# Kernel optimization log

Hardware: AMD Instinct MI355X
Metric: run time of the kernel (lower is better)

Reference implementation:

```python
import jax, jax.numpy as jnp
import numpy as np

RATE = 22050.0 / 256.0
_RANGES = [(0.0, 0.32537674), (0.32537674, 0.47555801), (0.47555801, 0.64588683),
           (0.64588683, 1.16883525), (1.16883525, 2.17128976), (2.17128976, np.inf)]
LO = np.array([a * RATE for a, _ in _RANGES], dtype=np.float32)
HI = np.array([b * RATE for _, b in _RANGES], dtype=np.float32)
WEIGHT = 1.0
EPS = 1e-7


def _giou1d(a0, a1, b0, b1):
    # 1D GIoU between intervals [a0,a1] (GT) and [b0,b1] (pred)
    inter = jnp.clip(jnp.minimum(a1, b1) - jnp.maximum(a0, b0), 0.0)
    union = (a1 - a0) + (b1 - b0) - inter
    enclose = jnp.maximum(a1, b1) - jnp.minimum(a0, b0)
    iou = inter / (union + EPS)
    return iou - (enclose - union) / (enclose + EPS)


def _fcos_loss(regressions, annotations, anchor_levels):
    # anchor_levels: list of 6 1D point arrays. All annotations are valid and
    # belong to class_id, so the boolean class filters are identity (jit-safe).
    def per_sample(reg, ann):
        # sort GTs by interval length ascending (as in get_fcos_positives)
        order = jnp.argsort(ann[:, 1] - ann[:, 0])
        ann = ann[order]  # [G, 3]
        losses, pos_masks = [], []
        off = 0
        for i, pts in enumerate(anchor_levels):
            n = pts.shape[0]
            reg_i = reg[off:off + n]  # [n, 2]
            off += n
            l_star = pts[None, :] - ann[:, 0:1]   # [G, n]
            r_star = ann[:, 1:2] - pts[None, :]   # [G, n]
            in_box = (l_star >= 0.0) & (r_star >= 0.0)
            m = jnp.maximum(l_star, r_star)
            mask = in_box & (m >= LO[i]) & (m < HI[i])  # [G, n]
            pos = mask.any(axis=0)                 # [n]
            arg = jnp.argmax(mask, axis=0)         # first matching GT per anchor
            norm_ann = ann[arg] / (2.0 ** i)       # [n, 3] normalized annotation
            giou = _giou1d(norm_ann[:, 0], norm_ann[:, 1], reg_i[:, 0], reg_i[:, 1])
            losses.append(1.0 - giou)
            pos_masks.append(pos)
        loss = jnp.concatenate(losses)            # [A]
        pos = jnp.concatenate(pos_masks)          # [A]
        cnt = jnp.maximum(pos.sum(), 1)
        return (loss * pos).sum() / cnt * WEIGHT  # mean over positive anchors
    return jax.vmap(per_sample)(regressions, annotations)


def setup_inputs() -> dict:
    key = jax.random.key(0)
    k0, k1, k2, k3 = jax.random.split(key, 4)
    B, G, L = 8, 256, 16384
    levels = [L >> i for i in range(6)]  # 16384..512, total 32256
    A = sum(levels)
    anchors = {f"anchors_l{i}": (jnp.arange(n, dtype=jnp.float32) * float(2 ** i))
               for i, n in enumerate(levels)}
    start = jax.random.uniform(k0, (B, G), minval=0.0, maxval=float(L) - 500.0)
    length = jax.random.uniform(k1, (B, G), minval=20.0, maxval=400.0)
    annotations = jnp.stack([start, start + length, jnp.zeros((B, G))], axis=-1)
    p0 = jax.random.uniform(k2, (B, A), minval=0.0, maxval=float(L))
    w = jax.random.uniform(k3, (B, A), minval=1.0, maxval=400.0)
    regressions = jnp.stack([p0, p0 + w], axis=-1)
    out = {"regressions": regressions, "annotations": annotations, "class_id": 0}
    out.update(anchors)
    return out


def reference(regressions, annotations, anchors_l0, anchors_l1, anchors_l2,
              anchors_l3, anchors_l4, anchors_l5, class_id):
    if class_id == -1:
        raise ValueError
    anchor_levels = [anchors_l0, anchors_l1, anchors_l2, anchors_l3, anchors_l4, anchors_l5]
    return _fcos_loss(regressions, annotations, anchor_levels)
```

## Files before the change

### kernel.cpp

```cpp
#include <hip/hip_runtime.h>
#include <math.h>

#define BATCH 8
#define G 256
#define A_TOT 32256
#define NCHUNK 126
#define BLKS_PER_S 32
#define GRID_BLKS (BATCH * BLKS_PER_S)
#define MAGIC 0x5A17C0DE5A17C0DEull

__constant__ float c_LO[6] = {
    0.0f,
    (float)(0.32537674 * (22050.0 / 256.0)),
    (float)(0.47555801 * (22050.0 / 256.0)),
    (float)(0.64588683 * (22050.0 / 256.0)),
    (float)(1.16883525 * (22050.0 / 256.0)),
    (float)(2.17128976 * (22050.0 / 256.0)),
};
__constant__ float c_HI[6] = {
    (float)(0.32537674 * (22050.0 / 256.0)),
    (float)(0.47555801 * (22050.0 / 256.0)),
    (float)(0.64588683 * (22050.0 / 256.0)),
    (float)(1.16883525 * (22050.0 / 256.0)),
    (float)(2.17128976 * (22050.0 / 256.0)),
    INFINITY,
};

__device__ __forceinline__ void scan_pair(
    const float4 v, const int j, const float p, const float lo, const float hi,
    float& bLen, int& bIdx, float& b0, float& b1)
{
    const float la = p - v.x, ra = v.y - p;
    const float ma = fmaxf(la, ra);
    const float lenA = v.y - v.x;
    if ((fminf(la, ra) >= 0.f) & (ma >= lo) & (ma < hi) & (lenA < bLen)) {
        bLen = lenA; bIdx = j; b0 = v.x; b1 = v.y;
    }
    const float lb = p - v.z, rb = v.w - p;
    const float mb = fmaxf(lb, rb);
    const float lenB = v.w - v.z;
    if ((fminf(lb, rb) >= 0.f) & (mb >= lo) & (mb < hi) & (lenB < bLen)) {
        bLen = lenB; bIdx = j + 1; b0 = v.z; b1 = v.w;
    }
}

__global__ __launch_bounds__(256) void fcos_persist_kernel(
    const float* __restrict__ reg,
    const float* __restrict__ ann,
    float2* __restrict__ partial,
    unsigned long long* __restrict__ flag,
    float* __restrict__ out)
{
    const int bid  = blockIdx.x;
    const int b    = bid >> 5;
    const int c    = bid & 31;
    const int t    = threadIdx.x;
    const int lane = t & 63;
    const int wid  = t >> 6;

    __shared__ __align__(16) float2 s_cpair[G + 4];
    __shared__ int   s_wcnt[4];
    __shared__ float s_wl[4], s_wc[4];

    const float a0in = ann[(b * G + t) * 3 + 0];
    const float a1in = ann[(b * G + t) * 3 + 1];
    const float len  = a1in - a0in;

    float lossAcc = 0.f, cntAcc = 0.f;

    for (int cc = c; cc < NCHUNK; cc += BLKS_PER_S) {
        const int aidx0 = cc * 256;
        int lvl, off;
        if (aidx0 < 16384)      { lvl = 0; off = 0; }
        else if (aidx0 < 24576) { lvl = 1; off = 16384; }
        else if (aidx0 < 28672) { lvl = 2; off = 24576; }
        else if (aidx0 < 30720) { lvl = 3; off = 28672; }
        else if (aidx0 < 31744) { lvl = 4; off = 30720; }
        else                    { lvl = 5; off = 31744; }

        const float lo  = c_LO[lvl];
        const float hi  = c_HI[lvl];
        const float xlo = lo - 0.01f;
        const float xhi = 2.0f * hi + 0.01f;
        const float sc  = (float)(1 << lvl);

        const float P0 = (float)(aidx0 - off) * sc;
        const float P1 = (float)(aidx0 - off + 255) * sc;

        const int   aidx = aidx0 + t;
        const float p    = (float)(aidx - off) * sc;
        const float2 rv  = reinterpret_cast<const float2*>(reg)[b * A_TOT + aidx];

        const bool cand = (len >= xlo) && (len < xhi) &&
                          (a1in >= P0 - 0.01f) && (a0in <= P1 + 0.01f);
        const unsigned long long vote = __ballot(cand);
        const int lanePos = __popcll(vote & ((1ull << lane) - 1ull));
        if (lane == 0) s_wcnt[wid] = __popcll(vote);
        __syncthreads();

        int base = 0, ncand = 0;
#pragma unroll
        for (int w = 0; w < 4; ++w) {
            const int n = s_wcnt[w];
            ncand += n;
            if (w < wid) base += n;
        }
        if (cand) s_cpair[base + lanePos] = make_float2(a0in, a1in);
        if (t < 4) s_cpair[ncand + t] = make_float2(3.0e30f, -3.0e30f);
        __syncthreads();

        float lenA = 1.0e30f, lenB = 1.0e30f;
        int   idxA = 0x7FFFFFFF, idxB = 0x7FFFFFFF;
        float a0A = 0.f, a1A = 0.f, a0B = 0.f, a1B = 0.f;
        const int n4 = (ncand + 3) >> 2;
        const float4* pr4 = reinterpret_cast<const float4*>(s_cpair);
        for (int g = 0; g < n4; ++g) {
            const float4 va = pr4[2 * g + 0];
            const float4 vb = pr4[2 * g + 1];
            scan_pair(va, 4 * g + 0, p, lo, hi, lenA, idxA, a0A, a1A);
            scan_pair(vb, 4 * g + 2, p, lo, hi, lenB, idxB, a0B, a1B);
        }
        const bool pickB = (lenB < lenA) || ((lenB == lenA) && (idxB < idxA));
        const float bLen = pickB ? lenB : lenA;
        const float bA0  = pickB ? a0B  : a0A;
        const float bA1  = pickB ? a1B  : a1A;

        if (bLen < 1.0e30f) {
            const float scale = 1.0f / sc;
            const float a0 = bA0 * scale;
            const float a1 = bA1 * scale;
            const float inter = fmaxf(fminf(a1, rv.y) - fmaxf(a0, rv.x), 0.f);
            const float uni   = (a1 - a0) + (rv.y - rv.x) - inter;
            const float enc   = fmaxf(a1, rv.y) - fminf(a0, rv.x);
            const float iou   = inter / (uni + 1e-7f);
            const float giou  = iou - (enc - uni) / (enc + 1e-7f);
            lossAcc += 1.0f - giou;
            cntAcc  += 1.0f;
        }
    }

#pragma unroll
    for (int m = 32; m; m >>= 1) {
        lossAcc += __shfl_xor(lossAcc, m);
        cntAcc  += __shfl_xor(cntAcc, m);
    }
    if (lane == 0) { s_wl[wid] = lossAcc; s_wc[wid] = cntAcc; }
    __syncthreads();
    if (t == 0) {
        const float L = s_wl[0] + s_wl[1] + s_wl[2] + s_wl[3];
        const float C = s_wc[0] + s_wc[1] + s_wc[2] + s_wc[3];
        partial[bid] = make_float2(L, C);
        __hip_atomic_store(&flag[bid], MAGIC, __ATOMIC_RELEASE, __HIP_MEMORY_SCOPE_AGENT);
    }

    if (c == 29 && wid == 0) {
        if (lane < BLKS_PER_S) {
            while (__hip_atomic_load(&flag[b * BLKS_PER_S + lane], __ATOMIC_ACQUIRE,
                                     __HIP_MEMORY_SCOPE_AGENT) != MAGIC) { }
        }
        float L = 0.f, C = 0.f;
        if (lane < BLKS_PER_S) {
            const float2 v = partial[b * BLKS_PER_S + lane];
            L = v.x; C = v.y;
        }
#pragma unroll
        for (int m = 32; m; m >>= 1) { L += __shfl_xor(L, m); C += __shfl_xor(C, m); }
        if (lane == 0) out[b] = L / fmaxf(C, 1.0f);
    }
}

extern "C" void kernel_launch(void* const* d_in, const int* in_sizes, int n_in,
                              void* d_out, int out_size, void* d_ws, size_t ws_size,
                              hipStream_t stream) {
    const float* reg = (const float*)d_in[0];
    const float* ann = (const float*)d_in[1];
    float* out = (float*)d_out;

    float2* partial = (float2*)d_ws;
    unsigned long long* flag =
        (unsigned long long*)((char*)d_ws + GRID_BLKS * sizeof(float2));

    fcos_persist_kernel<<<GRID_BLKS, 256, 0, stream>>>(reg, ann, partial, flag, out);
}
```

Measured before the change: 14.74 us.

## Prefetch inputs up front, use per-wave candidate segments and double buffers

Loads the batch's annotation block into shared memory with float4 reads and issues all regression loads for the block's chunks before the loop. Each wave now compacts its candidates into its own shared segment, with the segments double-buffered, which removes the cross-wave prefix sum and one barrier per chunk. The scan now keeps a single running best in strict order instead of two interleaved ones that had to be merged. It also moves the finalizer role to block 31. The costs are more shared memory and a serial scan across four segments, each padded to a multiple of four entries.

```diff
diff --git a/kernel.cpp b/kernel.cpp
--- a/kernel.cpp
+++ b/kernel.cpp
@@ -7,6 +7,7 @@
 #define NCHUNK 126
 #define BLKS_PER_S 32
 #define GRID_BLKS (BATCH * BLKS_PER_S)
+#define SEG 68
 #define MAGIC 0x5A17C0DE5A17C0DEull
 
 __constant__ float c_LO[6] = {
@@ -26,21 +27,25 @@
     INFINITY,
 };
 
-__device__ __forceinline__ void scan_pair(
-    const float4 v, const int j, const float p, const float lo, const float hi,
-    float& bLen, int& bIdx, float& b0, float& b1)
+__device__ __forceinline__ void scan4(
+    const float4 va, const float4 vb, const float p, const float lo, const float hi,
+    float& bLen, float& b0, float& b1)
 {
-    const float la = p - v.x, ra = v.y - p;
-    const float ma = fmaxf(la, ra);
-    const float lenA = v.y - v.x;
-    if ((fminf(la, ra) >= 0.f) & (ma >= lo) & (ma < hi) & (lenA < bLen)) {
-        bLen = lenA; bIdx = j; b0 = v.x; b1 = v.y;
+    {
+        const float l = p - va.x, r = va.y - p, m = fmaxf(l, r), ln = va.y - va.x;
+        if ((fminf(l, r) >= 0.f) & (m >= lo) & (m < hi) & (ln < bLen)) { bLen = ln; b0 = va.x; b1 = va.y; }
     }
-    const float lb = p - v.z, rb = v.w - p;
-    const float mb = fmaxf(lb, rb);
-    const float lenB = v.w - v.z;
-    if ((fminf(lb, rb) >= 0.f) & (mb >= lo) & (mb < hi) & (lenB < bLen)) {
-        bLen = lenB; bIdx = j + 1; b0 = v.z; b1 = v.w;
+    {
+        const float l = p - va.z, r = va.w - p, m = fmaxf(l, r), ln = va.w - va.z;
+        if ((fminf(l, r) >= 0.f) & (m >= lo) & (m < hi) & (ln < bLen)) { bLen = ln; b0 = va.z; b1 = va.w; }
+    }
+    {
+        const float l = p - vb.x, r = vb.y - p, m = fmaxf(l, r), ln = vb.y - vb.x;
+        if ((fminf(l, r) >= 0.f) & (m >= lo) & (m < hi) & (ln < bLen)) { bLen = ln; b0 = vb.x; b1 = vb.y; }
+    }
+    {
+        const float l = p - vb.z, r = vb.w - p, m = fmaxf(l, r), ln = vb.w - vb.z;
+        if ((fminf(l, r) >= 0.f) & (m >= lo) & (m < hi) & (ln < bLen)) { bLen = ln; b0 = vb.z; b1 = vb.w; }
     }
 }
 
@@ -58,17 +63,37 @@
     const int lane = t & 63;
     const int wid  = t >> 6;
 
-    __shared__ __align__(16) float2 s_cpair[G + 4];
-    __shared__ int   s_wcnt[4];
+    __shared__ __align__(16) float4 s_raw[G * 3 / 4];
+    __shared__ __align__(16) float2 s_cpair[2][4 * SEG];
+    __shared__ int   s_wcnt[2][4];
     __shared__ float s_wl[4], s_wc[4];
 
-    const float a0in = ann[(b * G + t) * 3 + 0];
-    const float a1in = ann[(b * G + t) * 3 + 1];
+    const float* annb = ann + b * (G * 3);
+    if (t < G * 3 / 4) s_raw[t] = reinterpret_cast<const float4*>(annb)[t];
+
+    const int nch = (c < 30) ? 4 : 3;
+    const float2* rg = reinterpret_cast<const float2*>(reg) + b * A_TOT;
+    const float2 rv0 = rg[(c +  0) * 256 + t];
+    const float2 rv1 = rg[(c + 32) * 256 + t];
+    const float2 rv2 = rg[(c + 64) * 256 + t];
+    const float2 rv3 = (nch == 4) ? rg[(c + 96) * 256 + t] : make_float2(0.f, 0.f);
+
+    __syncthreads();
+
+    const float* sf = reinterpret_cast<const float*>(s_raw);
+    const float a0in = sf[3 * t];
+    const float a1in = sf[3 * t + 1];
     const float len  = a1in - a0in;
 
     float lossAcc = 0.f, cntAcc = 0.f;
 
-    for (int cc = c; cc < NCHUNK; cc += BLKS_PER_S) {
+#pragma unroll
+    for (int k = 0; k < 4; ++k) {
+        if (k >= nch) break;
+        const int cc  = c + 32 * k;
+        const int buf = k & 1;
+        const float2 rv = (k == 0) ? rv0 : (k == 1) ? rv1 : (k == 2) ? rv2 : rv3;
+
         const int aidx0 = cc * 256;
         int lvl, off;
         if (aidx0 < 16384)      { lvl = 0; off = 0; }
@@ -83,47 +108,31 @@
         const float xlo = lo - 0.01f;
         const float xhi = 2.0f * hi + 0.01f;
         const float sc  = (float)(1 << lvl);
-
-        const float P0 = (float)(aidx0 - off) * sc;
-        const float P1 = (float)(aidx0 - off + 255) * sc;
-
-        const int   aidx = aidx0 + t;
-        const float p    = (float)(aidx - off) * sc;
-        const float2 rv  = reinterpret_cast<const float2*>(reg)[b * A_TOT + aidx];
+        const float P0  = (float)(aidx0 - off) * sc;
+        const float P1  = (float)(aidx0 - off + 255) * sc;
+        const float p   = (float)(aidx0 + t - off) * sc;
 
         const bool cand = (len >= xlo) && (len < xhi) &&
                           (a1in >= P0 - 0.01f) && (a0in <= P1 + 0.01f);
         const unsigned long long vote = __ballot(cand);
-        const int lanePos = __popcll(vote & ((1ull << lane) - 1ull));
-        if (lane == 0) s_wcnt[wid] = __popcll(vote);
+        const int cntw = __popcll(vote);
+        if (lane == 0) s_wcnt[buf][wid] = cntw;
+        const int pos = __popcll(vote & ((1ull << lane) - 1ull));
+        if (cand) s_cpair[buf][wid * SEG + pos] = make_float2(a0in, a1in);
+        if (lane < 4) s_cpair[buf][wid * SEG + cntw + lane] = make_float2(3.0e30f, -3.0e30f);
         __syncthreads();
 
-        int base = 0, ncand = 0;
+        float bLen = 1.0e30f, bA0 = 0.f, bA1 = 0.f;
 #pragma unroll
         for (int w = 0; w < 4; ++w) {
-            const int n = s_wcnt[w];
-            ncand += n;
-            if (w < wid) base += n;
+            const int nw = s_wcnt[buf][w];
+            const float4* seg4 = reinterpret_cast<const float4*>(&s_cpair[buf][w * SEG]);
+            for (int j = 0; j < nw; j += 4) {
+                const float4 va = seg4[(j >> 1) + 0];
+                const float4 vb = seg4[(j >> 1) + 1];
+                scan4(va, vb, p, lo, hi, bLen, bA0, bA1);
+            }
         }
-        if (cand) s_cpair[base + lanePos] = make_float2(a0in, a1in);
-        if (t < 4) s_cpair[ncand + t] = make_float2(3.0e30f, -3.0e30f);
-        __syncthreads();
-
-        float lenA = 1.0e30f, lenB = 1.0e30f;
-        int   idxA = 0x7FFFFFFF, idxB = 0x7FFFFFFF;
-        float a0A = 0.f, a1A = 0.f, a0B = 0.f, a1B = 0.f;
-        const int n4 = (ncand + 3) >> 2;
-        const float4* pr4 = reinterpret_cast<const float4*>(s_cpair);
-        for (int g = 0; g < n4; ++g) {
-            const float4 va = pr4[2 * g + 0];
-            const float4 vb = pr4[2 * g + 1];
-            scan_pair(va, 4 * g + 0, p, lo, hi, lenA, idxA, a0A, a1A);
-            scan_pair(vb, 4 * g + 2, p, lo, hi, lenB, idxB, a0B, a1B);
-        }
-        const bool pickB = (lenB < lenA) || ((lenB == lenA) && (idxB < idxA));
-        const float bLen = pickB ? lenB : lenA;
-        const float bA0  = pickB ? a0B  : a0A;
-        const float bA1  = pickB ? a1B  : a1A;
 
         if (bLen < 1.0e30f) {
             const float scale = 1.0f / sc;
@@ -153,7 +162,7 @@
         __hip_atomic_store(&flag[bid], MAGIC, __ATOMIC_RELEASE, __HIP_MEMORY_SCOPE_AGENT);
     }
 
-    if (c == 29 && wid == 0) {
+    if (c == 31 && wid == 0) {
         if (lane < BLKS_PER_S) {
             while (__hip_atomic_load(&flag[b * BLKS_PER_S + lane], __ATOMIC_ACQUIRE,
                                      __HIP_MEMORY_SCOPE_AGENT) != MAGIC) { }
```

New measurement: 14.35 us. 2.7% less time.
